# Performance work log

Hardware: AMD Instinct MI355X
Metric: run time of the kernel (lower is better)

Reference implementation:

```python
import jax, jax.numpy as jnp
import numpy as np


def gather_nodes(x, E_idx):
    # x: [B, N, C], E_idx: [B, N, K] -> x_j: [B, N, K, C]
    B, N, C = x.shape
    K = E_idx.shape[-1]
    idx = E_idx.reshape(B, N * K, 1)                      # [B, N*K, 1]
    x_j = jnp.take_along_axis(x, idx, axis=1)             # [B, N*K, C] (idx broadcasts over C)
    return x_j.reshape(B, N, K, C)


def setup_inputs() -> dict:
    key = jax.random.key(0)
    ks = jax.random.split(key, 6)
    B, N, K = 4, 4096, 30
    C = 64          # num_filters == node feature dim
    E = 300         # edge_dim
    x = jax.random.normal(ks[0], (B, N, C), dtype=jnp.float32)
    edge_features = jax.random.normal(ks[1], (B, N, K, E), dtype=jnp.float32)
    E_idx = jax.random.randint(ks[2], (B, N, K), 0, N, dtype=jnp.int64)
    W1 = jax.random.normal(ks[3], (E, C), dtype=jnp.float32) * (1.0 / np.sqrt(E))
    b1 = jnp.zeros((C,), dtype=jnp.float32)
    W2 = jax.random.normal(ks[4], (C, C), dtype=jnp.float32) * (1.0 / np.sqrt(C))
    b2 = jnp.zeros((C,), dtype=jnp.float32)
    return {"x": x, "edge_features": edge_features, "E_idx": E_idx,
            "W1": W1, "b1": b1, "W2": W2, "b2": b2}


def reference(x, edge_features, E_idx, W1, b1, W2, b2):
    # Filter network: Linear -> GELU -> Linear -> GELU (torch GELU is exact/erf)
    h = jax.nn.gelu(edge_features @ W1 + b1, approximate=False)   # [B,N,K,C]
    W = jax.nn.gelu(h @ W2 + b2, approximate=False)               # [B,N,K,C]
    x_j = gather_nodes(x, E_idx)                                  # [B,N,K,C]
    x_conv = jnp.sum(x_j * W, axis=2)                             # [B,N,C]
    return x_conv
```

## Files before the change

kernel.cpp:

```cpp
#include <hip/hip_runtime.h>


typedef __bf16 bf16x8 __attribute__((ext_vector_type(8)));
typedef float f32x4 __attribute__((ext_vector_type(4)));

#define B_    4
#define N_    4096
#define K_    30
#define C_    64
#define E_    300
#define EPAD  320

__device__ __forceinline__ float gelu_exact(float v) {
    return 0.5f * v * (1.0f + erff(v * 0.70710678118654752440f));
}

__global__ __launch_bounds__(256, 2) void cfconv_kernel(
    const float* __restrict__ x,
    const float* __restrict__ ef,
    const int*   __restrict__ eidx,
    const float* __restrict__ W1,
    const float* __restrict__ b1,
    const float* __restrict__ W2,
    const float* __restrict__ b2,
    float*       __restrict__ out,
    int nquads)
{
    __shared__ __align__(16) __bf16 Bt[64 * EPAD];
    __shared__ __align__(16) __bf16 W2t[64 * 64];
    __shared__ __align__(16) __bf16 Hb[128 * 64];

    const int tid = threadIdx.x;
    const int w   = tid >> 6;
    const int l   = tid & 63;
    const int m16 = l & 15;
    const int q   = l >> 4;

    for (int e = tid; e < 64 * EPAD; e += 256) {
        int k = e >> 6, n = e & 63;
        float v = (k < E_) ? W1[k * 64 + n] : 0.0f;
        int lb = k >> 3;
        int pb = (lb & ~7) | ((lb & 7) ^ (n & 7));
        Bt[n * EPAD + pb * 8 + (k & 7)] = (__bf16)v;
    }
    for (int e = tid; e < 64 * 64; e += 256) {
        int k = e >> 6, n = e & 63;
        int pb = (k >> 3) ^ (n & 7);
        W2t[n * 64 + pb * 8 + (k & 7)] = (__bf16)W2[k * 64 + n];
    }
    float b1v[4], b2v[4];
#pragma unroll
    for (int ct = 0; ct < 4; ++ct) {
        b1v[ct] = b1[ct * 16 + m16];
        b2v[ct] = b2[ct * 16 + m16];
    }
    __syncthreads();

    __bf16* hw = &Hb[w * 32 * 64];

    for (int quad = blockIdx.x; quad < nquads; quad += gridDim.x) {
        const int gq = quad * 4 + w;
        const float* efg = ef + (size_t)gq * (K_ * E_);

        f32x4 acc1[2][4];
#pragma unroll
        for (int rt = 0; rt < 2; ++rt)
#pragma unroll
            for (int ct = 0; ct < 4; ++ct)
                acc1[rt][ct] = (f32x4){0.f, 0.f, 0.f, 0.f};

#pragma unroll
        for (int kc = 0; kc < 5; ++kc) {
            bf16x8 af[2][2];
#pragma unroll
            for (int rt = 0; rt < 2; ++rt) {
                int r = rt * 16 + m16;
#pragma unroll
                for (int kh = 0; kh < 2; ++kh) {
                    int k0 = kc * 64 + kh * 32 + q * 8;
                    f32x4 v0 = (f32x4){0.f, 0.f, 0.f, 0.f};
                    f32x4 v1 = (f32x4){0.f, 0.f, 0.f, 0.f};
                    if (r < K_ && k0 < E_) {
                        const float* p = efg + r * E_ + k0;
                        v0 = *(const f32x4*)p;
                        if (k0 + 4 < E_) v1 = *(const f32x4*)(p + 4);
                    }
                    bf16x8 a;
                    a[0] = (__bf16)v0[0]; a[1] = (__bf16)v0[1];
                    a[2] = (__bf16)v0[2]; a[3] = (__bf16)v0[3];
                    a[4] = (__bf16)v1[0]; a[5] = (__bf16)v1[1];
                    a[6] = (__bf16)v1[2]; a[7] = (__bf16)v1[3];
                    af[rt][kh] = a;
                }
            }
            bf16x8 bfr[4][2];
#pragma unroll
            for (int ct = 0; ct < 4; ++ct) {
                int n = ct * 16 + m16;
#pragma unroll
                for (int kh = 0; kh < 2; ++kh) {
                    int lb = kc * 8 + kh * 4 + q;
                    int pb = (lb & ~7) | ((lb & 7) ^ (n & 7));
                    bfr[ct][kh] = *(const bf16x8*)&Bt[n * EPAD + pb * 8];
                }
            }
#pragma unroll
            for (int kh = 0; kh < 2; ++kh)
#pragma unroll
                for (int rt = 0; rt < 2; ++rt)
#pragma unroll
                    for (int ct = 0; ct < 4; ++ct)
                        acc1[rt][ct] = __builtin_amdgcn_mfma_f32_16x16x32_bf16(
                            af[rt][kh], bfr[ct][kh], acc1[rt][ct], 0, 0, 0);
        }

#pragma unroll
        for (int rt = 0; rt < 2; ++rt)
#pragma unroll
            for (int ct = 0; ct < 4; ++ct)
#pragma unroll
                for (int reg = 0; reg < 4; ++reg) {
                    int r = rt * 16 + q * 4 + reg;
                    int c = ct * 16 + m16;
                    float hv = gelu_exact(acc1[rt][ct][reg] + b1v[ct]);
                    hw[r * 64 + (((c >> 3) ^ (r & 7)) << 3) + (c & 7)] = (__bf16)hv;
                }

        f32x4 acc2[2][4];
#pragma unroll
        for (int rt = 0; rt < 2; ++rt)
#pragma unroll
            for (int ct = 0; ct < 4; ++ct)
                acc2[rt][ct] = (f32x4){0.f, 0.f, 0.f, 0.f};

        bf16x8 ah[2][2];
#pragma unroll
        for (int rt = 0; rt < 2; ++rt) {
            int m = rt * 16 + m16;
#pragma unroll
            for (int kh = 0; kh < 2; ++kh) {
                int lb = kh * 4 + q;
                ah[rt][kh] = *(const bf16x8*)&hw[m * 64 + ((lb ^ (m & 7)) << 3)];
            }
        }
        bf16x8 bw[4][2];
#pragma unroll
        for (int ct = 0; ct < 4; ++ct) {
            int n = ct * 16 + m16;
#pragma unroll
            for (int kh = 0; kh < 2; ++kh) {
                int lb = kh * 4 + q;
                bw[ct][kh] = *(const bf16x8*)&W2t[n * 64 + ((lb ^ (n & 7)) << 3)];
            }
        }
#pragma unroll
        for (int kh = 0; kh < 2; ++kh)
#pragma unroll
            for (int rt = 0; rt < 2; ++rt)
#pragma unroll
                for (int ct = 0; ct < 4; ++ct)
                    acc2[rt][ct] = __builtin_amdgcn_mfma_f32_16x16x32_bf16(
                        ah[rt][kh], bw[ct][kh], acc2[rt][ct], 0, 0, 0);

        const int bb = gq >> 12;
        const int* ig = eidx + gq * K_;
        const float* xb = x + (size_t)bb * (N_ * C_);
        float s[4] = {0.f, 0.f, 0.f, 0.f};
#pragma unroll
        for (int rt = 0; rt < 2; ++rt)
#pragma unroll
            for (int reg = 0; reg < 4; ++reg) {
                int r = rt * 16 + q * 4 + reg;
                if (r < K_) {
                    int idx = ig[r];
                    const float* xr = xb + idx * C_;
#pragma unroll
                    for (int ct = 0; ct < 4; ++ct) {
                        float wv = gelu_exact(acc2[rt][ct][reg] + b2v[ct]);
                        s[ct] = fmaf(wv, xr[ct * 16 + m16], s[ct]);
                    }
                }
            }
#pragma unroll
        for (int ct = 0; ct < 4; ++ct) {
            s[ct] += __shfl_xor(s[ct], 16, 64);
            s[ct] += __shfl_xor(s[ct], 32, 64);
        }
        float vout = (q == 0) ? s[0] : (q == 1) ? s[1] : (q == 2) ? s[2] : s[3];
        out[(size_t)gq * C_ + l] = vout;
    }
}

extern "C" void kernel_launch(void* const* d_in, const int* in_sizes, int n_in,
                              void* d_out, int out_size, void* d_ws, size_t ws_size,
                              hipStream_t stream) {
    const float* x   = (const float*)d_in[0];
    const float* ef  = (const float*)d_in[1];
    const int*   idx = (const int*)d_in[2];
    const float* W1  = (const float*)d_in[3];
    const float* b1  = (const float*)d_in[4];
    const float* W2  = (const float*)d_in[5];
    const float* b2  = (const float*)d_in[6];
    float* out = (float*)d_out;

    const int nquads = (B_ * N_) / 4;
    dim3 grid(512), block(256);
    hipLaunchKernelGGL(cfconv_kernel, grid, block, 0, stream,
                       x, ef, idx, W1, b1, W2, b2, out, nquads);
}
```

Baseline: 934.5 us.

## Transpose first GEMM, fold bias into weights, shuffle H between GEMMs, raise occupancy

Computes the first GEMM as W1^T times edge features, so the bf16 result already sits in registers in a layout that lane shuffles can turn into the second GEMM's A operand. This removes the shared-memory H staging buffer and its writes and reads. The b1 bias is folded into padded row 300 of W1, with a 1.0 injected into the edge-feature operand. Edge loads drop their bounds checks by reading past row ends into the next group's data; the last group reads a workspace copy of itself so it does not run past the buffer. Neighbor indices are loaded once per lane and broadcast by shuffle, launch bounds go to 3 blocks per SM and the grid grows to 768, at the cost of an extra device memcpy per launch and more shuffle work.

```diff
diff --git a/kernel.cpp b/kernel.cpp
--- a/kernel.cpp
+++ b/kernel.cpp
@@ -2,7 +2,9 @@
 
 
 typedef __bf16 bf16x8 __attribute__((ext_vector_type(8)));
-typedef float f32x4 __attribute__((ext_vector_type(4)));
+typedef __bf16 bf16x2 __attribute__((ext_vector_type(2)));
+typedef float  f32x4  __attribute__((ext_vector_type(4)));
+typedef unsigned int u32x4 __attribute__((ext_vector_type(4)));
 
 #define B_    4
 #define N_    4096
@@ -10,12 +12,14 @@
 #define C_    64
 #define E_    300
 #define EPAD  320
+#define NG    (B_ * N_)
+#define WPB   4
 
 __device__ __forceinline__ float gelu_exact(float v) {
     return 0.5f * v * (1.0f + erff(v * 0.70710678118654752440f));
 }
 
-__global__ __launch_bounds__(256, 2) void cfconv_kernel(
+__global__ __launch_bounds__(256, 3) void cfconv_kernel(
     const float* __restrict__ x,
     const float* __restrict__ ef,
     const int*   __restrict__ eidx,
@@ -23,12 +27,11 @@
     const float* __restrict__ b1,
     const float* __restrict__ W2,
     const float* __restrict__ b2,
-    float*       __restrict__ out,
-    int nquads)
+    const float* __restrict__ ef_tail,
+    float*       __restrict__ out)
 {
     __shared__ __align__(16) __bf16 Bt[64 * EPAD];
     __shared__ __align__(16) __bf16 W2t[64 * 64];
-    __shared__ __align__(16) __bf16 Hb[128 * 64];
 
     const int tid = threadIdx.x;
     const int w   = tid >> 6;
@@ -38,7 +41,7 @@
 
     for (int e = tid; e < 64 * EPAD; e += 256) {
         int k = e >> 6, n = e & 63;
-        float v = (k < E_) ? W1[k * 64 + n] : 0.0f;
+        float v = (k < E_) ? W1[k * 64 + n] : ((k == E_) ? b1[n] : 0.0f);
         int lb = k >> 3;
         int pb = (lb & ~7) | ((lb & 7) ^ (n & 7));
         Bt[n * EPAD + pb * 8 + (k & 7)] = (__bf16)v;
@@ -48,83 +51,94 @@
         int pb = (k >> 3) ^ (n & 7);
         W2t[n * 64 + pb * 8 + (k & 7)] = (__bf16)W2[k * 64 + n];
     }
-    float b1v[4], b2v[4];
-#pragma unroll
-    for (int ct = 0; ct < 4; ++ct) {
-        b1v[ct] = b1[ct * 16 + m16];
-        b2v[ct] = b2[ct * 16 + m16];
-    }
+    float b2v[4];
+#pragma unroll
+    for (int ct = 0; ct < 4; ++ct) b2v[ct] = b2[ct * 16 + m16];
     __syncthreads();
 
-    __bf16* hw = &Hb[w * 32 * 64];
-
-    for (int quad = blockIdx.x; quad < nquads; quad += gridDim.x) {
-        const int gq = quad * 4 + w;
-        const float* efg = ef + (size_t)gq * (K_ * E_);
-
-        f32x4 acc1[2][4];
-#pragma unroll
-        for (int rt = 0; rt < 2; ++rt)
-#pragma unroll
-            for (int ct = 0; ct < 4; ++ct)
-                acc1[rt][ct] = (f32x4){0.f, 0.f, 0.f, 0.f};
+    for (int g = blockIdx.x * WPB + w; g < NG; g += gridDim.x * WPB) {
+        const float* efg = (g == NG - 1) ? ef_tail
+                                         : ef + (size_t)g * (K_ * E_);
+        int iv = eidx[g * K_ + (l < K_ ? l : K_ - 1)];
+
+        f32x4 acc1[4][2];
+#pragma unroll
+        for (int mt = 0; mt < 4; ++mt)
+#pragma unroll
+            for (int nt = 0; nt < 2; ++nt)
+                acc1[mt][nt] = (f32x4){0.f, 0.f, 0.f, 0.f};
 
 #pragma unroll
         for (int kc = 0; kc < 5; ++kc) {
-            bf16x8 af[2][2];
-#pragma unroll
-            for (int rt = 0; rt < 2; ++rt) {
-                int r = rt * 16 + m16;
+            bf16x8 bfe[2][2];
+#pragma unroll
+            for (int nt = 0; nt < 2; ++nt) {
+                const float* pr = efg + (nt * 16 + m16) * E_;
 #pragma unroll
                 for (int kh = 0; kh < 2; ++kh) {
-                    int k0 = kc * 64 + kh * 32 + q * 8;
-                    f32x4 v0 = (f32x4){0.f, 0.f, 0.f, 0.f};
-                    f32x4 v1 = (f32x4){0.f, 0.f, 0.f, 0.f};
-                    if (r < K_ && k0 < E_) {
-                        const float* p = efg + r * E_ + k0;
-                        v0 = *(const f32x4*)p;
-                        if (k0 + 4 < E_) v1 = *(const f32x4*)(p + 4);
-                    }
+                    const float* p = pr + kc * 64 + kh * 32 + q * 8;
+                    f32x4 v0 = *(const f32x4*)p;
+                    f32x4 v1 = *(const f32x4*)(p + 4);
                     bf16x8 a;
                     a[0] = (__bf16)v0[0]; a[1] = (__bf16)v0[1];
                     a[2] = (__bf16)v0[2]; a[3] = (__bf16)v0[3];
                     a[4] = (__bf16)v1[0]; a[5] = (__bf16)v1[1];
                     a[6] = (__bf16)v1[2]; a[7] = (__bf16)v1[3];
-                    af[rt][kh] = a;
-                }
-            }
-            bf16x8 bfr[4][2];
-#pragma unroll
-            for (int ct = 0; ct < 4; ++ct) {
-                int n = ct * 16 + m16;
+                    bfe[nt][kh] = a;
+                }
+            }
+            if (kc == 4) {
+#pragma unroll
+                for (int nt = 0; nt < 2; ++nt)
+                    bfe[nt][1][4] = (q == 1) ? (__bf16)1.0f : bfe[nt][1][4];
+            }
+#pragma unroll
+            for (int mt = 0; mt < 4; ++mt) {
+                int n = mt * 16 + m16;
 #pragma unroll
                 for (int kh = 0; kh < 2; ++kh) {
                     int lb = kc * 8 + kh * 4 + q;
                     int pb = (lb & ~7) | ((lb & 7) ^ (n & 7));
-                    bfr[ct][kh] = *(const bf16x8*)&Bt[n * EPAD + pb * 8];
-                }
-            }
-#pragma unroll
-            for (int kh = 0; kh < 2; ++kh)
-#pragma unroll
-                for (int rt = 0; rt < 2; ++rt)
-#pragma unroll
-                    for (int ct = 0; ct < 4; ++ct)
-                        acc1[rt][ct] = __builtin_amdgcn_mfma_f32_16x16x32_bf16(
-                            af[rt][kh], bfr[ct][kh], acc1[rt][ct], 0, 0, 0);
+                    bf16x8 aw = *(const bf16x8*)&Bt[n * EPAD + pb * 8];
+#pragma unroll
+                    for (int nt = 0; nt < 2; ++nt)
+                        acc1[mt][nt] = __builtin_amdgcn_mfma_f32_16x16x32_bf16(
+                            aw, bfe[nt][kh], acc1[mt][nt], 0, 0, 0);
+                }
+            }
         }
 
+        unsigned pk[4][2][2];
+#pragma unroll
+        for (int mt = 0; mt < 4; ++mt)
+#pragma unroll
+            for (int nt = 0; nt < 2; ++nt) {
+                bf16x2 p0, p1;
+                p0[0] = (__bf16)gelu_exact(acc1[mt][nt][0]);
+                p0[1] = (__bf16)gelu_exact(acc1[mt][nt][1]);
+                p1[0] = (__bf16)gelu_exact(acc1[mt][nt][2]);
+                p1[1] = (__bf16)gelu_exact(acc1[mt][nt][3]);
+                pk[mt][nt][0] = __builtin_bit_cast(unsigned, p0);
+                pk[mt][nt][1] = __builtin_bit_cast(unsigned, p1);
+            }
+
+        const int sel  = q >> 1;
+        const int base = (q & 1) * 2;
+        bf16x8 af2[2][2];
 #pragma unroll
         for (int rt = 0; rt < 2; ++rt)
 #pragma unroll
-            for (int ct = 0; ct < 4; ++ct)
-#pragma unroll
-                for (int reg = 0; reg < 4; ++reg) {
-                    int r = rt * 16 + q * 4 + reg;
-                    int c = ct * 16 + m16;
-                    float hv = gelu_exact(acc1[rt][ct][reg] + b1v[ct]);
-                    hw[r * 64 + (((c >> 3) ^ (r & 7)) << 3) + (c & 7)] = (__bf16)hv;
-                }
+            for (int kh = 0; kh < 2; ++kh) {
+                u32x4 d;
+#pragma unroll
+                for (int t = 0; t < 4; ++t) {
+                    int srclane = (base + (t >> 1)) * 16 + m16;
+                    int lo = __shfl((int)pk[2 * kh][rt][t & 1], srclane, 64);
+                    int hi = __shfl((int)pk[2 * kh + 1][rt][t & 1], srclane, 64);
+                    d[t] = (unsigned)(sel ? hi : lo);
+                }
+                af2[rt][kh] = __builtin_bit_cast(bf16x8, d);
+            }
 
         f32x4 acc2[2][4];
 #pragma unroll
@@ -132,38 +146,21 @@
 #pragma unroll
             for (int ct = 0; ct < 4; ++ct)
                 acc2[rt][ct] = (f32x4){0.f, 0.f, 0.f, 0.f};
-
-        bf16x8 ah[2][2];
-#pragma unroll
-        for (int rt = 0; rt < 2; ++rt) {
-            int m = rt * 16 + m16;
+#pragma unroll
+        for (int ct = 0; ct < 4; ++ct) {
+            int n = ct * 16 + m16;
 #pragma unroll
             for (int kh = 0; kh < 2; ++kh) {
                 int lb = kh * 4 + q;
-                ah[rt][kh] = *(const bf16x8*)&hw[m * 64 + ((lb ^ (m & 7)) << 3)];
+                bf16x8 bw = *(const bf16x8*)&W2t[n * 64 + ((lb ^ (n & 7)) << 3)];
+#pragma unroll
+                for (int rt = 0; rt < 2; ++rt)
+                    acc2[rt][ct] = __builtin_amdgcn_mfma_f32_16x16x32_bf16(
+                        af2[rt][kh], bw, acc2[rt][ct], 0, 0, 0);
             }
         }
-        bf16x8 bw[4][2];
-#pragma unroll
-        for (int ct = 0; ct < 4; ++ct) {
-            int n = ct * 16 + m16;
-#pragma unroll
-            for (int kh = 0; kh < 2; ++kh) {
-                int lb = kh * 4 + q;
-                bw[ct][kh] = *(const bf16x8*)&W2t[n * 64 + ((lb ^ (n & 7)) << 3)];
-            }
-        }
-#pragma unroll
-        for (int kh = 0; kh < 2; ++kh)
-#pragma unroll
-            for (int rt = 0; rt < 2; ++rt)
-#pragma unroll
-                for (int ct = 0; ct < 4; ++ct)
-                    acc2[rt][ct] = __builtin_amdgcn_mfma_f32_16x16x32_bf16(
-                        ah[rt][kh], bw[ct][kh], acc2[rt][ct], 0, 0, 0);
-
-        const int bb = gq >> 12;
-        const int* ig = eidx + gq * K_;
+
+        const int bb = g >> 12;
         const float* xb = x + (size_t)bb * (N_ * C_);
         float s[4] = {0.f, 0.f, 0.f, 0.f};
 #pragma unroll
@@ -171,14 +168,14 @@
 #pragma unroll
             for (int reg = 0; reg < 4; ++reg) {
                 int r = rt * 16 + q * 4 + reg;
-                if (r < K_) {
-                    int idx = ig[r];
-                    const float* xr = xb + idx * C_;
-#pragma unroll
-                    for (int ct = 0; ct < 4; ++ct) {
-                        float wv = gelu_exact(acc2[rt][ct][reg] + b2v[ct]);
-                        s[ct] = fmaf(wv, xr[ct * 16 + m16], s[ct]);
-                    }
+                int idx = __shfl(iv, r, 64);
+                const float* xr = xb + (size_t)idx * C_;
+                bool valid = (r < K_);
+#pragma unroll
+                for (int ct = 0; ct < 4; ++ct) {
+                    float wv = gelu_exact(acc2[rt][ct][reg] + b2v[ct]);
+                    wv = valid ? wv : 0.0f;
+                    s[ct] = fmaf(wv, xr[ct * 16 + m16], s[ct]);
                 }
             }
 #pragma unroll
@@ -187,7 +184,7 @@
             s[ct] += __shfl_xor(s[ct], 32, 64);
         }
         float vout = (q == 0) ? s[0] : (q == 1) ? s[1] : (q == 2) ? s[2] : s[3];
-        out[(size_t)gq * C_ + l] = vout;
+        out[(size_t)g * C_ + l] = vout;
     }
 }
 
@@ -203,8 +200,11 @@
     const float* b2  = (const float*)d_in[6];
     float* out = (float*)d_out;
 
-    const int nquads = (B_ * N_) / 4;
-    dim3 grid(512), block(256);
+    hipMemcpyAsync(d_ws, ef + (size_t)(NG - 1) * (K_ * E_),
+                   (size_t)(K_ * E_) * sizeof(float),
+                   hipMemcpyDeviceToDevice, stream);
+
+    dim3 grid(768), block(256);
     hipLaunchKernelGGL(cfconv_kernel, grid, block, 0, stream,
-                       x, ef, idx, W1, b1, W2, b2, out, nquads);
+                       x, ef, idx, W1, b1, W2, b2, (const float*)d_ws, out);
 }
```

Measured after the change: 939.4 us. No clear change (+0.5%).
